# Kernel tuning notes

Hardware: AMD Instinct MI355X
Metric: run time of the kernel (lower is better)

Reference implementation:

```python
import jax, jax.numpy as jnp
import numpy as np

B, CIN, COUT, H, W = 8, 64, 64, 256, 256
M1, M2, NPROD = 16, 16, 4
COUT_LIN = COUT - NPROD  # 60
SCALE = 1.0 / (CIN * COUT)


def setup_inputs() -> dict:
    key = jax.random.key(0)
    ks = jax.random.split(key, 5)
    wshape = (CIN, COUT_LIN, M1, M2)
    return {
        "x": jax.random.normal(ks[0], (B, CIN, H, W), dtype=jnp.float32),
        "w1r": SCALE * jax.random.uniform(ks[1], wshape, dtype=jnp.float32),
        "w1i": SCALE * jax.random.uniform(ks[2], wshape, dtype=jnp.float32),
        "w2r": SCALE * jax.random.uniform(ks[3], wshape, dtype=jnp.float32),
        "w2i": SCALE * jax.random.uniform(ks[4], wshape, dtype=jnp.float32),
    }


def reference(x, w1r, w1i, w2r, w2i):
    b, c, h, w = x.shape
    wf = w // 2 + 1  # rfft width
    w1 = w1r + 1j * w1i
    w2 = w2r + 1j * w2i

    x_ft = jnp.fft.rfft2(x)  # [b, c, h, wf] complex64

    # mode-truncated channel mixing on low / high frequency blocks
    low = jnp.einsum("bixy,ioxy->boxy", x_ft[:, :, :M1, :M2], w1)
    high = jnp.einsum("bixy,ioxy->boxy", x_ft[:, :, h - M1:, :M2], w2)

    out_ft = jnp.zeros((b, COUT_LIN, h, wf), dtype=x_ft.dtype)
    out_ft = out_ft.at[:, :, :M1, :M2].set(low)
    out_ft = out_ft.at[:, :, h - M1:, :M2].set(high)

    # product path: complex pairwise products of adjacent channels
    prod = out_ft[:, 0:2 * NPROD:2] * out_ft[:, 1:2 * NPROD:2]  # [b, NPROD, h, wf]
    out_ft_full = jnp.concatenate([out_ft, prod], axis=1)  # [b, COUT, h, wf]

    return jnp.fft.irfft2(out_ft_full, s=(h, w))  # [b, COUT, h, w] real
```

## Files before the change

### kernel.cpp

```cpp
#include <hip/hip_runtime.h>

#define TWOPI_256 0.024543692606170259f

__global__ __launch_bounds__(256) void k1_fwd(const float* __restrict__ x,
                                              float2* __restrict__ Xm) {
  const int blk = blockIdx.x;
  const int tid = threadIdx.x;

  __shared__ float tabc[256];
  __shared__ float tabs[256];
  __shared__ float xT[16][256];
  __shared__ float Pbf[8704];

  {
    float s, c;
    sincosf((float)tid * TWOPI_256, &s, &c);
    tabc[tid] = c;
    tabs[tid] = s;
  }

  const int hg = tid >> 2;
  const int kg = tid & 3;

  float accr[4][4], acci[4][4];
#pragma unroll
  for (int i = 0; i < 4; ++i)
#pragma unroll
    for (int j = 0; j < 4; ++j) { accr[i][j] = 0.f; acci[i][j] = 0.f; }

  const float4* xrow = (const float4*)(x + ((size_t)blk << 16) + tid * 256);
  float4 vld[4];
#pragma unroll
  for (int q = 0; q < 4; ++q) vld[q] = xrow[q];

  __syncthreads();

  float cr[4], sr[4];
#pragma unroll
  for (int j = 0; j < 4; ++j) {
    const int k = kg * 4 + j;
    cr[j] = tabc[k];
    sr[j] = tabs[k];
  }

  for (int wc = 0; wc < 16; ++wc) {
    __syncthreads();
#pragma unroll
    for (int q = 0; q < 4; ++q) {
      xT[q * 4 + 0][tid] = vld[q].x;
      xT[q * 4 + 1][tid] = vld[q].y;
      xT[q * 4 + 2][tid] = vld[q].z;
      xT[q * 4 + 3][tid] = vld[q].w;
    }
    if (wc < 15) {
#pragma unroll
      for (int q = 0; q < 4; ++q) vld[q] = xrow[(wc + 1) * 4 + q];
    }
    __syncthreads();

    const int w0 = wc * 16;
    float c[4], s[4];
#pragma unroll
    for (int j = 0; j < 4; ++j) {
      const int idx = ((kg * 4 + j) * w0) & 255;
      c[j] = tabc[idx];
      s[j] = tabs[idx];
    }
#pragma unroll 4
    for (int wi = 0; wi < 16; ++wi) {
      const float4 xv = *(const float4*)&xT[wi][hg * 4];
#pragma unroll
      for (int j = 0; j < 4; ++j) {
        accr[0][j] += xv.x * c[j]; acci[0][j] -= xv.x * s[j];
        accr[1][j] += xv.y * c[j]; acci[1][j] -= xv.y * s[j];
        accr[2][j] += xv.z * c[j]; acci[2][j] -= xv.z * s[j];
        accr[3][j] += xv.w * c[j]; acci[3][j] -= xv.w * s[j];
        const float cn = c[j] * cr[j] - s[j] * sr[j];
        const float sn = s[j] * cr[j] + c[j] * sr[j];
        c[j] = cn; s[j] = sn;
      }
    }
  }

#pragma unroll
  for (int j = 0; j < 4; ++j) {
    const int k = kg * 4 + j;
    const int base = k * 544 + 4 * (k & 7) + 8 * hg;
    *(float4*)&Pbf[base]     = make_float4(accr[0][j], acci[0][j], accr[1][j], acci[1][j]);
    *(float4*)&Pbf[base + 4] = make_float4(accr[2][j], acci[2][j], accr[3][j], acci[3][j]);
  }
  __syncthreads();

  const int k = tid & 15;
  const int tt = tid >> 4;
  const int pbase = k * 544 + 4 * (k & 7);
  float c0 = 1.f, s0 = 0.f, c1 = 1.f, s1 = 0.f;
  const float cr0 = tabc[tt], sr0 = tabs[tt];
  const float cr1 = tabc[240 + tt], sr1 = tabs[240 + tt];
  float X0r = 0.f, X0i = 0.f, X1r = 0.f, X1i = 0.f;
  for (int h = 0; h < 256; h += 2) {
    const float4 pv = *(const float4*)&Pbf[pbase + 2 * h];
    X0r += pv.x * c0 + pv.y * s0; X0i += pv.y * c0 - pv.x * s0;
    X1r += pv.x * c1 + pv.y * s1; X1i += pv.y * c1 - pv.x * s1;
    float cn = c0 * cr0 - s0 * sr0, sn = s0 * cr0 + c0 * sr0; c0 = cn; s0 = sn;
    cn = c1 * cr1 - s1 * sr1; sn = s1 * cr1 + c1 * sr1; c1 = cn; s1 = sn;
    X0r += pv.z * c0 + pv.w * s0; X0i += pv.w * c0 - pv.z * s0;
    X1r += pv.z * c1 + pv.w * s1; X1i += pv.w * c1 - pv.z * s1;
    cn = c0 * cr0 - s0 * sr0; sn = s0 * cr0 + c0 * sr0; c0 = cn; s0 = sn;
    cn = c1 * cr1 - s1 * sr1; sn = s1 * cr1 + c1 * sr1; c1 = cn; s1 = sn;
  }
  const int ci = blk & 63, b = blk >> 6;
  Xm[((tt * 16 + k) * 64 + ci) * 8 + b]        = make_float2(X0r, X0i);
  Xm[(((tt + 16) * 16 + k) * 64 + ci) * 8 + b] = make_float2(X1r, X1i);
}

__global__ __launch_bounds__(256) void k2_mix(const float2* __restrict__ Xm,
                                              const float* __restrict__ w1r,
                                              const float* __restrict__ w1i,
                                              const float* __restrict__ w2r,
                                              const float* __restrict__ w2i,
                                              float2* __restrict__ Am) {
  const int blk = blockIdx.x;
  const int t = blk >> 4, k = blk & 15;
  const int tp = t & 15;
  const float* __restrict__ wr = (t < 16) ? w1r : w2r;
  const float* __restrict__ wi = (t < 16) ? w1i : w2i;
  const int tid = threadIdx.x;

  __shared__ float2 Xs[64][8];
  __shared__ float2 Cb[64][8];

  {
    const float2* src = Xm + ((size_t)blk << 9);
    float2* dst = &Xs[0][0];
    dst[tid] = src[tid];
    dst[tid + 256] = src[tid + 256];
  }
  __syncthreads();

  for (int n = tid; n < 480; n += 256) {
    const int o = n >> 3, bb = n & 7;
    const int wofs = o * 256 + tp * 16 + k;
    float ar = 0.f, ai = 0.f;
#pragma unroll 4
    for (int i = 0; i < 64; ++i) {
      const float wrv = wr[i * 15360 + wofs];
      const float wiv = wi[i * 15360 + wofs];
      const float2 xv = Xs[i][bb];
      ar += xv.x * wrv - xv.y * wiv;
      ai += xv.x * wiv + xv.y * wrv;
    }
    Cb[o][bb] = make_float2(ar, ai);
  }
  __syncthreads();
  if (tid < 32) {
    const int p = tid >> 3, bb = tid & 7;
    const float2 u = Cb[2 * p][bb], v = Cb[2 * p + 1][bb];
    Cb[60 + p][bb] = make_float2(u.x * v.x - u.y * v.y, u.x * v.y + u.y * v.x);
  }
  __syncthreads();
  const float alpha = (k == 0 ? 1.f : 2.f) * (1.f / 65536.f);
#pragma unroll
  for (int n = tid; n < 512; n += 256) {
    const int o = n >> 3, bb = n & 7;
    const float2 v = Cb[o][bb];
    Am[(((size_t)(bb * 64 + o)) * 32 + t) * 16 + k] = make_float2(v.x * alpha, v.y * alpha);
  }
}

__device__ __forceinline__ unsigned int bfp(float a) {
  return (__float_as_uint(a) + 0x8000u) >> 16;
}

__global__ __launch_bounds__(256) void k3_inv(const float2* __restrict__ Am,
                                              float* __restrict__ out) {
  const int blk = blockIdx.x;
  const int tid = threadIdx.x;

  __shared__ float tabc[256];
  __shared__ float tabs[256];
  __shared__ float2 Ams[32][16];
  __shared__ unsigned short Zt[32][264];
  __shared__ float Tt[10240];

  {
    float s, c;
    sincosf((float)tid * TWOPI_256, &s, &c);
    tabc[tid] = c;
    tabs[tid] = s;
  }
  {
    const float2* src = Am + ((size_t)blk << 9);
    float2* dst = &Ams[0][0];
    dst[tid] = src[tid];
    dst[tid + 256] = src[tid + 256];
  }
  __syncthreads();

#pragma unroll
  for (int j = 0; j < 32; ++j) {
    const int w = tid;
    const int idx = ((j >> 1) * w) & 255;
    const float val = (j & 1) ? -tabs[idx] : tabc[idx];
    Tt[j * 320 + (w >> 4) * 20 + (w & 15)] = val;
  }

  const int hg = tid >> 2, kg = tid & 3;
  float Zr[4][4], Zi[4][4];
#pragma unroll
  for (int i = 0; i < 4; ++i)
#pragma unroll
    for (int j = 0; j < 4; ++j) { Zr[i][j] = 0.f; Zi[i][j] = 0.f; }
  float ch[4], sh[4], crh[4], srh[4];
#pragma unroll
  for (int i = 0; i < 4; ++i) {
    const int h = hg * 4 + i;
    crh[i] = tabc[h];
    srh[i] = tabs[h];
    ch[i] = 1.f;
    sh[i] = 0.f;
  }
  for (int t = 0; t < 32; ++t) {
    if (t == 16) {
#pragma unroll
      for (int i = 0; i < 4; ++i) {
        const int idx = (240 * (hg * 4 + i)) & 255;
        ch[i] = tabc[idx];
        sh[i] = tabs[idx];
      }
    }
    const float4 a01 = *(const float4*)&Ams[t][kg * 4];
    const float4 a23 = *(const float4*)&Ams[t][kg * 4 + 2];
    const float Ar[4] = {a01.x, a01.z, a23.x, a23.z};
    const float Ai[4] = {a01.y, a01.w, a23.y, a23.w};
#pragma unroll
    for (int i = 0; i < 4; ++i) {
#pragma unroll
      for (int j = 0; j < 4; ++j) {
        Zr[i][j] += Ar[j] * ch[i] - Ai[j] * sh[i];
        Zi[i][j] += Ar[j] * sh[i] + Ai[j] * ch[i];
      }
      const float cn = ch[i] * crh[i] - sh[i] * srh[i];
      const float sn = sh[i] * crh[i] + ch[i] * srh[i];
      ch[i] = cn;
      sh[i] = sn;
    }
  }
#pragma unroll
  for (int j = 0; j < 4; ++j) {
    const int kk = kg * 4 + j;
    const unsigned int p0 = bfp(Zr[0][j]) | (bfp(Zr[1][j]) << 16);
    const unsigned int p1 = bfp(Zr[2][j]) | (bfp(Zr[3][j]) << 16);
    *(uint2*)&Zt[2 * kk][hg * 4] = make_uint2(p0, p1);
    const unsigned int q0 = bfp(Zi[0][j]) | (bfp(Zi[1][j]) << 16);
    const unsigned int q1 = bfp(Zi[2][j]) | (bfp(Zi[3][j]) << 16);
    *(uint2*)&Zt[2 * kk + 1][hg * 4] = make_uint2(q0, q1);
  }
  __syncthreads();

  const int wg = tid & 15, hg2 = tid >> 4;
  float* outp = out + ((size_t)blk << 16);
  for (int chunk = 0; chunk < 2; ++chunk) {
    const int h0 = chunk * 128 + hg2 * 8;
    float acc[8][16];
#pragma unroll
    for (int ii = 0; ii < 8; ++ii)
#pragma unroll
      for (int ww = 0; ww < 16; ++ww) acc[ii][ww] = 0.f;
    for (int j = 0; j < 32; ++j) {
      const uint4 zp = *(const uint4*)&Zt[j][h0];
      float zv[8];
      zv[0] = __uint_as_float(zp.x << 16);
      zv[1] = __uint_as_float(zp.x & 0xffff0000u);
      zv[2] = __uint_as_float(zp.y << 16);
      zv[3] = __uint_as_float(zp.y & 0xffff0000u);
      zv[4] = __uint_as_float(zp.z << 16);
      zv[5] = __uint_as_float(zp.z & 0xffff0000u);
      zv[6] = __uint_as_float(zp.w << 16);
      zv[7] = __uint_as_float(zp.w & 0xffff0000u);
      const float* tb = &Tt[j * 320 + wg * 20];
      const float4 t0 = *(const float4*)&tb[0];
      const float4 t1 = *(const float4*)&tb[4];
      const float4 t2 = *(const float4*)&tb[8];
      const float4 t3 = *(const float4*)&tb[12];
      const float tv[16] = {t0.x, t0.y, t0.z, t0.w, t1.x, t1.y, t1.z, t1.w,
                            t2.x, t2.y, t2.z, t2.w, t3.x, t3.y, t3.z, t3.w};
#pragma unroll
      for (int ii = 0; ii < 8; ++ii)
#pragma unroll
        for (int ww = 0; ww < 16; ++ww) acc[ii][ww] += zv[ii] * tv[ww];
    }
#pragma unroll
    for (int ii = 0; ii < 8; ++ii) {
      float* row = outp + (size_t)(h0 + ii) * 256 + wg * 16;
      *(float4*)&row[0]  = make_float4(acc[ii][0], acc[ii][1], acc[ii][2], acc[ii][3]);
      *(float4*)&row[4]  = make_float4(acc[ii][4], acc[ii][5], acc[ii][6], acc[ii][7]);
      *(float4*)&row[8]  = make_float4(acc[ii][8], acc[ii][9], acc[ii][10], acc[ii][11]);
      *(float4*)&row[12] = make_float4(acc[ii][12], acc[ii][13], acc[ii][14], acc[ii][15]);
    }
  }
}

extern "C" void kernel_launch(void* const* d_in, const int* in_sizes, int n_in,
                              void* d_out, int out_size, void* d_ws, size_t ws_size,
                              hipStream_t stream) {
  const float* x   = (const float*)d_in[0];
  const float* w1r = (const float*)d_in[1];
  const float* w1i = (const float*)d_in[2];
  const float* w2r = (const float*)d_in[3];
  const float* w2i = (const float*)d_in[4];
  float* out = (float*)d_out;

  float2* Xm = (float2*)d_ws;
  float2* Am = Xm + 262144;

  k1_fwd<<<dim3(512), dim3(256), 0, stream>>>(x, Xm);
  k2_mix<<<dim3(512), dim3(256), 0, stream>>>(Xm, w1r, w1i, w2r, w2i, Am);
  k3_inv<<<dim3(512), dim3(256), 0, stream>>>(Am, out);
}
```

Measured before the change: 371.6 us.

## Split forward DFT into two kernels and halve inverse-DFT block work

Splits the forward transform into a W-direction DFT kernel with 2048 blocks that reads rows straight from global memory, with no LDS transpose or barriers, and a separate H-direction DFT kernel that reads an intermediate buffer in workspace. The inverse kernel is split across twice as many blocks, each handling half the rows, and stores its twiddle table as bf16 to cut LDS footprint and register accumulators. The aim is more parallelism and occupancy on the many-CU device. In exchange it adds a kernel launch, a global round trip for the intermediate, and lower precision for the inverse twiddles.

```diff
diff --git a/kernel.cpp b/kernel.cpp
--- a/kernel.cpp
+++ b/kernel.cpp
@@ -2,116 +2,105 @@
 
 #define TWOPI_256 0.024543692606170259f
 
-__global__ __launch_bounds__(256) void k1_fwd(const float* __restrict__ x,
-                                              float2* __restrict__ Xm) {
+__global__ __launch_bounds__(256) void k1a_wdft(const float* __restrict__ x,
+                                                float2* __restrict__ Pg) {
   const int blk = blockIdx.x;
+  const int img = blk >> 2, hc = blk & 3;
   const int tid = threadIdx.x;
 
-  __shared__ float tabc[256];
-  __shared__ float tabs[256];
-  __shared__ float xT[16][256];
-  __shared__ float Pbf[8704];
-
+  __shared__ float tabc[256], tabs[256];
   {
     float s, c;
     sincosf((float)tid * TWOPI_256, &s, &c);
     tabc[tid] = c;
     tabs[tid] = s;
   }
-
-  const int hg = tid >> 2;
-  const int kg = tid & 3;
-
-  float accr[4][4], acci[4][4];
-#pragma unroll
-  for (int i = 0; i < 4; ++i)
-#pragma unroll
-    for (int j = 0; j < 4; ++j) { accr[i][j] = 0.f; acci[i][j] = 0.f; }
-
-  const float4* xrow = (const float4*)(x + ((size_t)blk << 16) + tid * 256);
-  float4 vld[4];
-#pragma unroll
-  for (int q = 0; q < 4; ++q) vld[q] = xrow[q];
-
-  __syncthreads();
-
-  float cr[4], sr[4];
-#pragma unroll
-  for (int j = 0; j < 4; ++j) {
-    const int k = kg * 4 + j;
-    cr[j] = tabc[k];
-    sr[j] = tabs[k];
-  }
+  __syncthreads();
+
+  const int k = tid & 15, rg = tid >> 4;
+  const int h0 = hc * 64 + rg * 4;
+  const float* rowp = x + ((size_t)img << 16) + (size_t)h0 * 256;
+  const float4* r0 = (const float4*)rowp;
+  const float4* r1 = (const float4*)(rowp + 256);
+  const float4* r2 = (const float4*)(rowp + 512);
+  const float4* r3 = (const float4*)(rowp + 768);
+
+  const float cr = tabc[k], sr = tabs[k];
+  float accr[4] = {0.f, 0.f, 0.f, 0.f}, acci[4] = {0.f, 0.f, 0.f, 0.f};
 
   for (int wc = 0; wc < 16; ++wc) {
-    __syncthreads();
-#pragma unroll
-    for (int q = 0; q < 4; ++q) {
-      xT[q * 4 + 0][tid] = vld[q].x;
-      xT[q * 4 + 1][tid] = vld[q].y;
-      xT[q * 4 + 2][tid] = vld[q].z;
-      xT[q * 4 + 3][tid] = vld[q].w;
-    }
-    if (wc < 15) {
-#pragma unroll
-      for (int q = 0; q < 4; ++q) vld[q] = xrow[(wc + 1) * 4 + q];
-    }
-    __syncthreads();
-
-    const int w0 = wc * 16;
-    float c[4], s[4];
-#pragma unroll
-    for (int j = 0; j < 4; ++j) {
-      const int idx = ((kg * 4 + j) * w0) & 255;
-      c[j] = tabc[idx];
-      s[j] = tabs[idx];
-    }
-#pragma unroll 4
-    for (int wi = 0; wi < 16; ++wi) {
-      const float4 xv = *(const float4*)&xT[wi][hg * 4];
-#pragma unroll
-      for (int j = 0; j < 4; ++j) {
-        accr[0][j] += xv.x * c[j]; acci[0][j] -= xv.x * s[j];
-        accr[1][j] += xv.y * c[j]; acci[1][j] -= xv.y * s[j];
-        accr[2][j] += xv.z * c[j]; acci[2][j] -= xv.z * s[j];
-        accr[3][j] += xv.w * c[j]; acci[3][j] -= xv.w * s[j];
-        const float cn = c[j] * cr[j] - s[j] * sr[j];
-        const float sn = s[j] * cr[j] + c[j] * sr[j];
-        c[j] = cn; s[j] = sn;
+    const int tw = (k * wc * 16) & 255;
+    float c = tabc[tw], s = tabs[tw];
+#pragma unroll
+    for (int sc = 0; sc < 4; ++sc) {
+      const int fi = wc * 4 + sc;
+      const float4 a0 = r0[fi], a1 = r1[fi], a2 = r2[fi], a3 = r3[fi];
+      const float xv[4][4] = {{a0.x, a1.x, a2.x, a3.x},
+                              {a0.y, a1.y, a2.y, a3.y},
+                              {a0.z, a1.z, a2.z, a3.z},
+                              {a0.w, a1.w, a2.w, a3.w}};
+#pragma unroll
+      for (int wi = 0; wi < 4; ++wi) {
+#pragma unroll
+        for (int i = 0; i < 4; ++i) {
+          accr[i] += xv[wi][i] * c;
+          acci[i] -= xv[wi][i] * s;
+        }
+        const float cn = c * cr - s * sr;
+        const float sn = s * cr + c * sr;
+        c = cn; s = sn;
       }
     }
   }
 
-#pragma unroll
-  for (int j = 0; j < 4; ++j) {
-    const int k = kg * 4 + j;
-    const int base = k * 544 + 4 * (k & 7) + 8 * hg;
-    *(float4*)&Pbf[base]     = make_float4(accr[0][j], acci[0][j], accr[1][j], acci[1][j]);
-    *(float4*)&Pbf[base + 4] = make_float4(accr[2][j], acci[2][j], accr[3][j], acci[3][j]);
-  }
-  __syncthreads();
-
-  const int k = tid & 15;
-  const int tt = tid >> 4;
-  const int pbase = k * 544 + 4 * (k & 7);
-  float c0 = 1.f, s0 = 0.f, c1 = 1.f, s1 = 0.f;
-  const float cr0 = tabc[tt], sr0 = tabs[tt];
-  const float cr1 = tabc[240 + tt], sr1 = tabs[240 + tt];
+  float2* dst = Pg + (size_t)((img * 16 + k) * 256 + h0);
+  *(float4*)dst       = make_float4(accr[0], acci[0], accr[1], acci[1]);
+  *(float4*)(dst + 2) = make_float4(accr[2], acci[2], accr[3], acci[3]);
+}
+
+__global__ __launch_bounds__(256) void k1b_hdft(const float2* __restrict__ Pg,
+                                                float2* __restrict__ Xm) {
+  const int img = blockIdx.x;
+  const int tid = threadIdx.x;
+
+  __shared__ float tabc[256], tabs[256];
+  __shared__ float2 Ps[16][258];
+
+  {
+    float s, c;
+    sincosf((float)tid * TWOPI_256, &s, &c);
+    tabc[tid] = c;
+    tabs[tid] = s;
+  }
+  {
+    const float4* src = (const float4*)(Pg + ((size_t)img << 12));
+#pragma unroll
+    for (int j = 0; j < 8; ++j) {
+      const int f = tid + j * 256;
+      const int kk = f >> 7, hp = (f & 127) << 1;
+      *(float4*)&Ps[kk][hp] = src[f];
+    }
+  }
+  __syncthreads();
+
+  const int t = tid >> 3, k2 = tid & 7;
+  const int kyv = (t < 16) ? t : (t + 224);
+  const float cr = tabc[kyv], sr = tabs[kyv];
+  float c = 1.f, s = 0.f;
   float X0r = 0.f, X0i = 0.f, X1r = 0.f, X1i = 0.f;
   for (int h = 0; h < 256; h += 2) {
-    const float4 pv = *(const float4*)&Pbf[pbase + 2 * h];
-    X0r += pv.x * c0 + pv.y * s0; X0i += pv.y * c0 - pv.x * s0;
-    X1r += pv.x * c1 + pv.y * s1; X1i += pv.y * c1 - pv.x * s1;
-    float cn = c0 * cr0 - s0 * sr0, sn = s0 * cr0 + c0 * sr0; c0 = cn; s0 = sn;
-    cn = c1 * cr1 - s1 * sr1; sn = s1 * cr1 + c1 * sr1; c1 = cn; s1 = sn;
-    X0r += pv.z * c0 + pv.w * s0; X0i += pv.w * c0 - pv.z * s0;
-    X1r += pv.z * c1 + pv.w * s1; X1i += pv.w * c1 - pv.z * s1;
-    cn = c0 * cr0 - s0 * sr0; sn = s0 * cr0 + c0 * sr0; c0 = cn; s0 = sn;
-    cn = c1 * cr1 - s1 * sr1; sn = s1 * cr1 + c1 * sr1; c1 = cn; s1 = sn;
-  }
-  const int ci = blk & 63, b = blk >> 6;
-  Xm[((tt * 16 + k) * 64 + ci) * 8 + b]        = make_float2(X0r, X0i);
-  Xm[(((tt + 16) * 16 + k) * 64 + ci) * 8 + b] = make_float2(X1r, X1i);
+    const float4 p0 = *(const float4*)&Ps[k2][h];
+    const float4 p1 = *(const float4*)&Ps[k2 + 8][h];
+    X0r += p0.x * c + p0.y * s; X0i += p0.y * c - p0.x * s;
+    X1r += p1.x * c + p1.y * s; X1i += p1.y * c - p1.x * s;
+    float cn = c * cr - s * sr, sn = s * cr + c * sr; c = cn; s = sn;
+    X0r += p0.z * c + p0.w * s; X0i += p0.w * c - p0.z * s;
+    X1r += p1.z * c + p1.w * s; X1i += p1.w * c - p1.z * s;
+    cn = c * cr - s * sr; sn = s * cr + c * sr; c = cn; s = sn;
+  }
+  const int ci = img & 63, b = img >> 6;
+  Xm[((t * 16 + k2) * 64 + ci) * 8 + b]     = make_float2(X0r, X0i);
+  Xm[((t * 16 + k2 + 8) * 64 + ci) * 8 + b] = make_float2(X1r, X1i);
 }
 
 __global__ __launch_bounds__(256) void k2_mix(const float2* __restrict__ Xm,
@@ -173,15 +162,15 @@
 }
 
 __global__ __launch_bounds__(256) void k3_inv(const float2* __restrict__ Am,
-                                              float* __restrict__ out) {
+                                             float* __restrict__ out) {
   const int blk = blockIdx.x;
+  const int bo = blk >> 1, hc = blk & 1, h0 = hc << 7;
   const int tid = threadIdx.x;
 
-  __shared__ float tabc[256];
-  __shared__ float tabs[256];
+  __shared__ float tabc[256], tabs[256];
   __shared__ float2 Ams[32][16];
-  __shared__ unsigned short Zt[32][264];
-  __shared__ float Tt[10240];
+  __shared__ unsigned short Zt[32][136];
+  __shared__ unsigned short Tt[32][264];
 
   {
     float s, c;
@@ -189,32 +178,26 @@
     tabc[tid] = c;
     tabs[tid] = s;
   }
-  {
-    const float2* src = Am + ((size_t)blk << 9);
-    float2* dst = &Ams[0][0];
-    dst[tid] = src[tid];
-    dst[tid + 256] = src[tid + 256];
-  }
+  ((float4*)&Ams[0][0])[tid] = ((const float4*)(Am + ((size_t)bo << 9)))[tid];
   __syncthreads();
 
 #pragma unroll
   for (int j = 0; j < 32; ++j) {
-    const int w = tid;
-    const int idx = ((j >> 1) * w) & 255;
+    const int idx = ((j >> 1) * tid) & 255;
     const float val = (j & 1) ? -tabs[idx] : tabc[idx];
-    Tt[j * 320 + (w >> 4) * 20 + (w & 15)] = val;
+    Tt[j][tid] = (unsigned short)bfp(val);
   }
 
   const int hg = tid >> 2, kg = tid & 3;
-  float Zr[4][4], Zi[4][4];
-#pragma unroll
-  for (int i = 0; i < 4; ++i)
+  float Zr[2][4], Zi[2][4];
+#pragma unroll
+  for (int i = 0; i < 2; ++i)
 #pragma unroll
     for (int j = 0; j < 4; ++j) { Zr[i][j] = 0.f; Zi[i][j] = 0.f; }
-  float ch[4], sh[4], crh[4], srh[4];
-#pragma unroll
-  for (int i = 0; i < 4; ++i) {
-    const int h = hg * 4 + i;
+  float ch[2], sh[2], crh[2], srh[2];
+#pragma unroll
+  for (int i = 0; i < 2; ++i) {
+    const int h = h0 + hg * 2 + i;
     crh[i] = tabc[h];
     srh[i] = tabs[h];
     ch[i] = 1.f;
@@ -223,8 +206,8 @@
   for (int t = 0; t < 32; ++t) {
     if (t == 16) {
 #pragma unroll
-      for (int i = 0; i < 4; ++i) {
-        const int idx = (240 * (hg * 4 + i)) & 255;
+      for (int i = 0; i < 2; ++i) {
+        const int idx = (240 * (h0 + hg * 2 + i)) & 255;
         ch[i] = tabc[idx];
         sh[i] = tabs[idx];
       }
@@ -234,7 +217,7 @@
     const float Ar[4] = {a01.x, a01.z, a23.x, a23.z};
     const float Ai[4] = {a01.y, a01.w, a23.y, a23.w};
 #pragma unroll
-    for (int i = 0; i < 4; ++i) {
+    for (int i = 0; i < 2; ++i) {
 #pragma unroll
       for (int j = 0; j < 4; ++j) {
         Zr[i][j] += Ar[j] * ch[i] - Ai[j] * sh[i];
@@ -249,26 +232,22 @@
 #pragma unroll
   for (int j = 0; j < 4; ++j) {
     const int kk = kg * 4 + j;
-    const unsigned int p0 = bfp(Zr[0][j]) | (bfp(Zr[1][j]) << 16);
-    const unsigned int p1 = bfp(Zr[2][j]) | (bfp(Zr[3][j]) << 16);
-    *(uint2*)&Zt[2 * kk][hg * 4] = make_uint2(p0, p1);
-    const unsigned int q0 = bfp(Zi[0][j]) | (bfp(Zi[1][j]) << 16);
-    const unsigned int q1 = bfp(Zi[2][j]) | (bfp(Zi[3][j]) << 16);
-    *(uint2*)&Zt[2 * kk + 1][hg * 4] = make_uint2(q0, q1);
+    *(unsigned int*)&Zt[2 * kk][2 * hg]     = bfp(Zr[0][j]) | (bfp(Zr[1][j]) << 16);
+    *(unsigned int*)&Zt[2 * kk + 1][2 * hg] = bfp(Zi[0][j]) | (bfp(Zi[1][j]) << 16);
   }
   __syncthreads();
 
   const int wg = tid & 15, hg2 = tid >> 4;
-  float* outp = out + ((size_t)blk << 16);
-  for (int chunk = 0; chunk < 2; ++chunk) {
-    const int h0 = chunk * 128 + hg2 * 8;
-    float acc[8][16];
+  float* outp = out + ((size_t)bo << 16);
+#pragma unroll
+  for (int wp = 0; wp < 2; ++wp) {
+    float acc[8][8];
 #pragma unroll
     for (int ii = 0; ii < 8; ++ii)
 #pragma unroll
-      for (int ww = 0; ww < 16; ++ww) acc[ii][ww] = 0.f;
+      for (int ww = 0; ww < 8; ++ww) acc[ii][ww] = 0.f;
     for (int j = 0; j < 32; ++j) {
-      const uint4 zp = *(const uint4*)&Zt[j][h0];
+      const uint4 zp = *(const uint4*)&Zt[j][hg2 * 8];
       float zv[8];
       zv[0] = __uint_as_float(zp.x << 16);
       zv[1] = __uint_as_float(zp.x & 0xffff0000u);
@@ -278,25 +257,26 @@
       zv[5] = __uint_as_float(zp.z & 0xffff0000u);
       zv[6] = __uint_as_float(zp.w << 16);
       zv[7] = __uint_as_float(zp.w & 0xffff0000u);
-      const float* tb = &Tt[j * 320 + wg * 20];
-      const float4 t0 = *(const float4*)&tb[0];
-      const float4 t1 = *(const float4*)&tb[4];
-      const float4 t2 = *(const float4*)&tb[8];
-      const float4 t3 = *(const float4*)&tb[12];
-      const float tv[16] = {t0.x, t0.y, t0.z, t0.w, t1.x, t1.y, t1.z, t1.w,
-                            t2.x, t2.y, t2.z, t2.w, t3.x, t3.y, t3.z, t3.w};
+      const uint4 tq = *(const uint4*)&Tt[j][wp * 128 + wg * 8];
+      float tv[8];
+      tv[0] = __uint_as_float(tq.x << 16);
+      tv[1] = __uint_as_float(tq.x & 0xffff0000u);
+      tv[2] = __uint_as_float(tq.y << 16);
+      tv[3] = __uint_as_float(tq.y & 0xffff0000u);
+      tv[4] = __uint_as_float(tq.z << 16);
+      tv[5] = __uint_as_float(tq.z & 0xffff0000u);
+      tv[6] = __uint_as_float(tq.w << 16);
+      tv[7] = __uint_as_float(tq.w & 0xffff0000u);
 #pragma unroll
       for (int ii = 0; ii < 8; ++ii)
 #pragma unroll
-        for (int ww = 0; ww < 16; ++ww) acc[ii][ww] += zv[ii] * tv[ww];
+        for (int ww = 0; ww < 8; ++ww) acc[ii][ww] += zv[ii] * tv[ww];
     }
 #pragma unroll
     for (int ii = 0; ii < 8; ++ii) {
-      float* row = outp + (size_t)(h0 + ii) * 256 + wg * 16;
-      *(float4*)&row[0]  = make_float4(acc[ii][0], acc[ii][1], acc[ii][2], acc[ii][3]);
-      *(float4*)&row[4]  = make_float4(acc[ii][4], acc[ii][5], acc[ii][6], acc[ii][7]);
-      *(float4*)&row[8]  = make_float4(acc[ii][8], acc[ii][9], acc[ii][10], acc[ii][11]);
-      *(float4*)&row[12] = make_float4(acc[ii][12], acc[ii][13], acc[ii][14], acc[ii][15]);
+      float* row = outp + (size_t)(h0 + hg2 * 8 + ii) * 256 + wp * 128 + wg * 8;
+      *(float4*)&row[0] = make_float4(acc[ii][0], acc[ii][1], acc[ii][2], acc[ii][3]);
+      *(float4*)&row[4] = make_float4(acc[ii][4], acc[ii][5], acc[ii][6], acc[ii][7]);
     }
   }
 }
@@ -313,8 +293,10 @@
 
   float2* Xm = (float2*)d_ws;
   float2* Am = Xm + 262144;
-
-  k1_fwd<<<dim3(512), dim3(256), 0, stream>>>(x, Xm);
+  float2* Pg = Am + 262144;
+
+  k1a_wdft<<<dim3(2048), dim3(256), 0, stream>>>(x, Pg);
+  k1b_hdft<<<dim3(512), dim3(256), 0, stream>>>(Pg, Xm);
   k2_mix<<<dim3(512), dim3(256), 0, stream>>>(Xm, w1r, w1i, w2r, w2i, Am);
-  k3_inv<<<dim3(512), dim3(256), 0, stream>>>(Am, out);
-}
+  k3_inv<<<dim3(1024), dim3(256), 0, stream>>>(Am, out);
+}
```

Result: slower. 400.7 us (+7.8%).
